# Optimization experiments

Measured on AMD Instinct MI355X. Metric: run time of the kernel, lower is better.

## Reference

```python
import jax, jax.numpy as jnp
import numpy as np

BN, BE, B = 50000, 800000, 16
NE, EE, GE, EH, NH = 32, 32, 32, 128, 128  # emb dims, hidden dims


def clean(x):
    return jnp.nan_to_num(x, nan=0.0, posinf=0.0, neginf=0.0)


def _lin(key, fan_in, fan_out):
    k1, k2 = jax.random.split(key)
    s = 1.0 / np.sqrt(fan_in)
    return (jax.random.uniform(k1, (fan_in, fan_out), jnp.float32, -s, s),
            jax.random.uniform(k2, (fan_out,), jnp.float32, -s, s))


def setup_inputs() -> dict:
    key = jax.random.key(0)
    ks = jax.random.split(key, 20)
    inp = {
        "x": jax.random.normal(ks[0], (BN, 2), jnp.float32),
        "edge_index": jax.random.randint(ks[1], (2, BE), 0, BN, jnp.int32),
        "batch": jax.random.randint(ks[2], (BN,), 0, B, jnp.int32),
        "node_attr": jnp.ones((BN, 2), jnp.float32),
        "edge_attr": jax.random.uniform(ks[3], (BE, 2), jnp.float32) + 0.5,  # positive spacings
        "glob_attr": jax.random.uniform(ks[4], (B, 2), jnp.float32),
    }
    # encoders (output 2*emb each, 'Duplicated')
    inp["enc_node_W"], inp["enc_node_b"] = _lin(ks[5], 2, 2 * NE)
    inp["enc_edge_W"], inp["enc_edge_b"] = _lin(ks[6], 2, 2 * EE)
    inp["enc_glob_W"], inp["enc_glob_b"] = _lin(ks[7], 2, 2 * GE)
    inp["enc2_W"], inp["enc2_b"] = _lin(ks[8], 2, 2 * EE)
    # derivative MLP: 4*NE+2*EE -> EH -> 2*EE
    inp["dW1"], inp["db1"] = _lin(ks[9], 4 * NE + 2 * EE, EH)
    inp["dW2"], inp["db2"] = _lin(ks[10], EH, 2 * EE)
    # half-jacobian MLP: 4*EE -> EH -> 2*EE
    inp["hW1"], inp["hb1"] = _lin(ks[11], 4 * EE, EH)
    inp["hW2"], inp["hb2"] = _lin(ks[12], EH, 2 * EE)
    # jacobian MLP: 6*EE -> NH -> 2*NE
    inp["jW1"], inp["jb1"] = _lin(ks[13], 6 * EE, NH)
    inp["jW2"], inp["jb2"] = _lin(ks[14], NH, 2 * NE)
    # hessian MLP: 4*EE+2*EE -> NH -> 2*NE
    inp["sW1"], inp["sb1"] = _lin(ks[15], 6 * EE, NH)
    inp["sW2"], inp["sb2"] = _lin(ks[16], NH, 2 * NE)
    # node MLP: 6*NE+2*GE -> NH -> 2*NE
    inp["nW1"], inp["nb1"] = _lin(ks[17], 6 * NE + 2 * GE, NH)
    inp["nW2"], inp["nb2"] = _lin(ks[18], NH, 2 * NE)
    # decoder: 2*NE -> 2
    inp["decW"], inp["decb"] = _lin(ks[19], 2 * NE, 2)
    return inp


def reference(x, edge_index, batch, node_attr, edge_attr, glob_attr,
              enc_node_W, enc_node_b, enc_edge_W, enc_edge_b, enc_glob_W, enc_glob_b,
              enc2_W, enc2_b,
              dW1, db1, dW2, db2,
              hW1, hb1, hW2, hb2,
              jW1, jb1, jW2, jb2,
              sW1, sb1, sW2, sb2,
              nW1, nb1, nW2, nb2,
              decW, decb):
    relu = jax.nn.relu
    seg = lambda d, idx: jax.ops.segment_sum(d, idx, num_segments=BN)
    mlp = lambda t, W1, b1, W2, b2: relu(t @ W1 + b1) @ W2 + b2

    row, col = edge_index[0], edge_index[1]
    spacing = edge_attr                                 # [BE,2]
    inv_spacing = clean(1.0 / spacing)
    inv_double = clean(1.0 / (seg(spacing, row) + seg(spacing, col)))  # [BN,2]

    node_emb = relu(x @ enc_node_W + enc_node_b)        # [BN,2*NE]
    spacing_emb = relu(spacing @ enc_edge_W + enc_edge_b)  # [BE,2*EE]
    glob_emb = relu(glob_attr @ enc_glob_W + enc_glob_b)   # [B,2*GE]
    inv_spacing_emb = relu(inv_spacing @ enc2_W + enc2_b)  # [BE,2*EE]
    inv_double_emb = relu(inv_double @ enc2_W + enc2_b)    # [BN,2*EE]

    d_edge = mlp(jnp.concatenate([node_emb[row], node_emb[col], inv_spacing_emb], -1),
                 dW1, db1, dW2, db2)                    # [BE,2*EE]
    hj_plus = seg(d_edge, row)                          # [BN,2*EE]
    hj_minus = seg(d_edge, col)

    jac1 = seg(mlp(jnp.concatenate([spacing_emb, hj_plus[col]], -1), hW1, hb1, hW2, hb2), col)
    jac2 = seg(mlp(jnp.concatenate([spacing_emb, hj_minus[row]], -1), hW1, hb1, hW2, hb2), row)
    jac = mlp(jnp.concatenate([jac1, jac2, inv_double_emb], -1), jW1, jb1, jW2, jb2)  # [BN,2*NE]

    hess = mlp(jnp.concatenate([hj_plus, hj_minus, inv_double_emb], -1), sW1, sb1, sW2, sb2)

    res = mlp(jnp.concatenate([node_emb, jac, glob_emb[batch], hess], -1), nW1, nb1, nW2, nb2)
    return node_attr * (res @ decW + decb)              # [BN,2]
```

## Files before the change

kernel.cpp:

```cpp
#include <hip/hip_runtime.h>
#include <hip/hip_fp16.h>
#include <math.h>

#define BN 50000
#define BE 800000
#define CHUNK 104

__device__ __forceinline__ float relu_f(float v) { return fmaxf(v, 0.0f); }
__device__ __forceinline__ float inv_clean(float s) {
    float q = 1.0f / s;
    return isfinite(q) ? q : 0.0f;
}
__device__ __forceinline__ float inv_clean_fast(float s) {
    float q = __builtin_amdgcn_rcpf(s);
    return isfinite(q) ? q : 0.0f;
}

__global__ __launch_bounds__(256) void k_pack_w1(
    const float* __restrict__ W, int r0, float4* __restrict__ dst)
{
    int t = blockIdx.x * 256 + threadIdx.x;
    if (t >= 2048) return;
    int j2 = t >> 6, l = t & 63;
    const float* ra = W + (size_t)(r0 + 2*j2) * 128 + 2*l;
    const float* rb = W + (size_t)(r0 + 2*j2 + 1) * 128 + 2*l;
    dst[t] = make_float4(ra[0], ra[1], rb[0], rb[1]);
}
__global__ __launch_bounds__(256) void k_pack_w2(
    const float* __restrict__ W2, float4* __restrict__ dst)
{
    int t = blockIdx.x * 256 + threadIdx.x;
    if (t >= 2048) return;
    int k4 = t >> 6, l = t & 63;
    dst[t] = make_float4(W2[(4*k4+0)*64+l], W2[(4*k4+1)*64+l],
                         W2[(4*k4+2)*64+l], W2[(4*k4+3)*64+l]);
}
__global__ __launch_bounds__(256) void k_pack_uv(
    const float* __restrict__ dW1, float4* __restrict__ dst)
{
    int t = blockIdx.x * 256 + threadIdx.x;
    if (t >= 4096) return;
    int j = t >> 6, l = t & 63;
    float4 w;
    if (l < 32) w = ((const float4*)(dW1 + (size_t)j*128))[l];
    else        w = ((const float4*)(dW1 + (size_t)(64+j)*128))[l-32];
    dst[t] = w;
}

__global__ __launch_bounds__(256) void k_hist_sumsp(
    const int* __restrict__ ei, const float* __restrict__ ea,
    int* __restrict__ rc, int* __restrict__ cc, float* __restrict__ sumsp)
{
    int e = blockIdx.x * 256 + threadIdx.x;
    if (e >= BE) return;
    int r = ei[e], c = ei[BE + e];
    atomicAdd(&rc[r], 1);
    atomicAdd(&cc[c], 1);
    float2 s = ((const float2*)ea)[e];
    atomicAdd(&sumsp[2*r],   s.x);
    atomicAdd(&sumsp[2*r+1], s.y);
    atomicAdd(&sumsp[2*c],   s.x);
    atomicAdd(&sumsp[2*c+1], s.y);
}

__global__ __launch_bounds__(1024) void k_scan(
    const int* __restrict__ cntR, int* __restrict__ hdR,
    const int* __restrict__ cntC, int* __restrict__ hdC)
{
    __shared__ int s[1024];
    const int* cnt; int* hd;
    if (blockIdx.x == 0) { cnt = cntR; hd = hdR; }
    else                 { cnt = cntC; hd = hdC; }
    int t = threadIdx.x;
    int base = t * 49;
    int sum = 0;
    for (int i = 0; i < 49; i++) {
        int idx = base + i;
        sum += (idx < BN) ? cnt[idx] : 0;
    }
    s[t] = sum;
    __syncthreads();
    for (int o = 1; o < 1024; o <<= 1) {
        int v = (t >= o) ? s[t - o] : 0;
        __syncthreads();
        s[t] += v;
        __syncthreads();
    }
    int run = s[t] - sum;
    for (int i = 0; i < 49; i++) {
        int idx = base + i;
        if (idx < BN) { hd[idx] = run; run += cnt[idx]; }
    }
}

__global__ __launch_bounds__(256) void k_scatter2(
    const int* __restrict__ ei, const float* __restrict__ ea,
    int* __restrict__ rhd, int* __restrict__ chd,
    int4* __restrict__ rs, int4* __restrict__ cs)
{
    int e = blockIdx.x * 256 + threadIdx.x;
    if (e >= BE) return;
    int r = ei[e], c = ei[BE + e];
    float2 s = ((const float2*)ea)[e];
    int s0 = __float_as_int(s.x), s1 = __float_as_int(s.y);
    int p1 = atomicAdd(&rhd[r], 1);
    rs[p1] = make_int4(r, c, s0, s1);
    int p2 = atomicAdd(&chd[c], 1);
    cs[p2] = make_int4(c, r, s0, s1);
}

__global__ __launch_bounds__(256, 6) void k_uvh(
    const float* __restrict__ x,
    const float* __restrict__ enW, const float* __restrict__ enB,
    const float4* __restrict__ guv,
    __half* __restrict__ u_h, __half* __restrict__ v_h)
{
    extern __shared__ float lds[];
    const int wid = threadIdx.x >> 6, l = threadIdx.x & 63;
    float4* xb4 = (float4*)(lds + wid * 512);
    const int gw = blockIdx.x * 4 + wid;
    const int nw = gridDim.x * 4;

    const int jj = l & 31;
    const float w0a = enW[jj],    w0b = enW[64+jj],  b0 = enB[jj];
    const float w1a = enW[jj+32], w1b = enW[96+jj],  b1 = enB[jj+32];

    for (int g = gw; g < BN/8; g += nw) {
        const int n0 = g * 8;
        const int q = l >> 5;
        {
            float2 xa = ((const float2*)x)[n0 + q*4 + 0];
            float2 xb = ((const float2*)x)[n0 + q*4 + 1];
            float2 xc = ((const float2*)x)[n0 + q*4 + 2];
            float2 xd = ((const float2*)x)[n0 + q*4 + 3];
            float4 p0, p1;
            p0.x = relu_f(fmaf(xa.x, w0a, fmaf(xa.y, w0b, b0)));
            p0.y = relu_f(fmaf(xb.x, w0a, fmaf(xb.y, w0b, b0)));
            p0.z = relu_f(fmaf(xc.x, w0a, fmaf(xc.y, w0b, b0)));
            p0.w = relu_f(fmaf(xd.x, w0a, fmaf(xd.y, w0b, b0)));
            p1.x = relu_f(fmaf(xa.x, w1a, fmaf(xa.y, w1b, b1)));
            p1.y = relu_f(fmaf(xb.x, w1a, fmaf(xb.y, w1b, b1)));
// ... 7 lines not shown
        for (int e = 0; e < 8; e++) acc[e] = make_float4(0,0,0,0);
        #pragma unroll 8
        for (int j = 0; j < 64; j++) {
            float4 wq = guv[j*64 + l];
            float4 xa = xb4[j*2 + 0];
            float4 xc = xb4[j*2 + 1];
            acc[0].x = fmaf(xa.x, wq.x, acc[0].x); acc[0].y = fmaf(xa.x, wq.y, acc[0].y);
            acc[0].z = fmaf(xa.x, wq.z, acc[0].z); acc[0].w = fmaf(xa.x, wq.w, acc[0].w);
            acc[1].x = fmaf(xa.y, wq.x, acc[1].x); acc[1].y = fmaf(xa.y, wq.y, acc[1].y);
            acc[1].z = fmaf(xa.y, wq.z, acc[1].z); acc[1].w = fmaf(xa.y, wq.w, acc[1].w);
            acc[2].x = fmaf(xa.z, wq.x, acc[2].x); acc[2].y = fmaf(xa.z, wq.y, acc[2].y);
            acc[2].z = fmaf(xa.z, wq.z, acc[2].z); acc[2].w = fmaf(xa.z, wq.w, acc[2].w);
            acc[3].x = fmaf(xa.w, wq.x, acc[3].x); acc[3].y = fmaf(xa.w, wq.y, acc[3].y);
            acc[3].z = fmaf(xa.w, wq.z, acc[3].z); acc[3].w = fmaf(xa.w, wq.w, acc[3].w);
            acc[4].x = fmaf(xc.x, wq.x, acc[4].x); acc[4].y = fmaf(xc.x, wq.y, acc[4].y);
            acc[4].z = fmaf(xc.x, wq.z, acc[4].z); acc[4].w = fmaf(xc.x, wq.w, acc[4].w);
            acc[5].x = fmaf(xc.y, wq.x, acc[5].x); acc[5].y = fmaf(xc.y, wq.y, acc[5].y);
            acc[5].z = fmaf(xc.y, wq.z, acc[5].z); acc[5].w = fmaf(xc.y, wq.w, acc[5].w);
            acc[6].x = fmaf(xc.z, wq.x, acc[6].x); acc[6].y = fmaf(xc.z, wq.y, acc[6].y);
            acc[6].z = fmaf(xc.z, wq.z, acc[6].z); acc[6].w = fmaf(xc.z, wq.w, acc[6].w);
            acc[7].x = fmaf(xc.w, wq.x, acc[7].x); acc[7].y = fmaf(xc.w, wq.y, acc[7].y);
            acc[7].z = fmaf(xc.w, wq.z, acc[7].z); acc[7].w = fmaf(xc.w, wq.w, acc[7].w);
        }
        __half* dst = (l < 32) ? (u_h + 4*l) : (v_h + 4*(l-32));
        #pragma unroll
        for (int e = 0; e < 8; e++) {
            __half2* p = (__half2*)(dst + (size_t)(n0+e)*128);
            p[0] = __floats2half2_rn(acc[e].x, acc[e].y);
            p[1] = __floats2half2_rn(acc[e].z, acc[e].w);
        }
    }
}

__global__ __launch_bounds__(256, 8) void k_e1s(
    const int4* __restrict__ rs,
    const __half* __restrict__ u_h, const __half* __restrict__ v_h,
    const float* __restrict__ e2w, const float* __restrict__ e2b,
    const float4* __restrict__ gw1, const float* __restrict__ db1,
    const float4* __restrict__ gw2, const float* __restrict__ db2,
    float* __restrict__ hjp, float* __restrict__ hjm)
{
    extern __shared__ float lds[];
    const int wid = threadIdx.x >> 6, l = threadIdx.x & 63;
    float* buf = lds + wid * 1024;
    float4* buf4 = (float4*)buf;

    const int jA = l >> 1;
    const int eh = l & 1;
    const float ewA0 = e2w[jA],      ewB0 = e2w[64+jA],    eb0v = e2b[jA];
    const float ewA1 = e2w[jA+32],   ewB1 = e2w[96+jA],    eb1v = e2b[jA+32];
    const float b1a = db1[2*l], b1b = db1[2*l+1];
    const float b2r = db2[l];

    const int wave = blockIdx.x * 4 + wid;
    const int start = wave * CHUNK;
    const int end = min(start + CHUNK, BE);

    float acc = 0.f;
    int cur = -1;

    for (int i = start; i < end; i += 8) {
        const int nact = min(8, end - i);
        int rr[8], cc[8];
        float2 spv[8];
        #pragma unroll
        for (int e = 0; e < 8; e++) {
            int idx = i + ((e < nact) ? e : nact - 1);
            int4 rec = rs[idx];
            rr[e] = rec.x; cc[e] = rec.y;
            spv[e] = make_float2(__int_as_float(rec.z), __int_as_float(rec.w));
        }
        {
            float2 sA = eh ? spv[4] : spv[0];
            float2 sB = eh ? spv[5] : spv[1];
            float2 sC = eh ? spv[6] : spv[2];
            float2 sD = eh ? spv[7] : spv[3];
            float qA0 = inv_clean_fast(sA.x), qA1 = inv_clean_fast(sA.y);
            float qB0 = inv_clean_fast(sB.x), qB1 = inv_clean_fast(sB.y);
            float qC0 = inv_clean_fast(sC.x), qC1 = inv_clean_fast(sC.y);
            float qD0 = inv_clean_fast(sD.x), qD1 = inv_clean_fast(sD.y);
            float4 p0, p1;
            p0.x = relu_f(fmaf(qA0, ewA0, fmaf(qA1, ewB0, eb0v)));
            p0.y = relu_f(fmaf(qB0, ewA0, fmaf(qB1, ewB0, eb0v)));
            p0.z = relu_f(fmaf(qC0, ewA0, fmaf(qC1, ewB0, eb0v)));
            p0.w = relu_f(fmaf(qD0, ewA0, fmaf(qD1, ewB0, eb0v)));
            p1.x = relu_f(fmaf(qA0, ewA1, fmaf(qA1, ewB1, eb1v)));
            p1.y = relu_f(fmaf(qB0, ewA1, fmaf(qB1, ewB1, eb1v)));
            p1.z = relu_f(fmaf(qC0, ewA1, fmaf(qC1, ewB1, eb1v)));
            p1.w = relu_f(fmaf(qD0, ewA1, fmaf(qD1, ewB1, eb1v)));
            buf4[jA*2 + eh]      = p0;
            buf4[(jA+32)*2 + eh] = p1;
        }

        float t0[8], t1[8];
        #pragma unroll
        for (int e = 0; e < 8; e++) {
            float2 uu = __half22float2(*(const __half2*)(u_h + (size_t)rr[e]*128 + 2*l));
            float2 vv = __half22float2(*(const __half2*)(v_h + (size_t)cc[e]*128 + 2*l));
            t0[e] = b1a + uu.x + vv.x;
            t1[e] = b1b + uu.y + vv.y;
        }

        #pragma unroll 8
        for (int j2 = 0; j2 < 32; j2++) {
            float4 wq = gw1[j2*64 + l];
            float4 xa = buf4[(2*j2)*2 + 0];
            float4 xbv = buf4[(2*j2)*2 + 1];
            float4 xc = buf4[(2*j2+1)*2 + 0];
            float4 xd = buf4[(2*j2+1)*2 + 1];
            t0[0] = fmaf(xa.x, wq.x, fmaf(xc.x, wq.z, t0[0]));
            t1[0] = fmaf(xa.x, wq.y, fmaf(xc.x, wq.w, t1[0]));
            t0[1] = fmaf(xa.y, wq.x, fmaf(xc.y, wq.z, t0[1]));
            t1[1] = fmaf(xa.y, wq.y, fmaf(xc.y, wq.w, t1[1]));
            t0[2] = fmaf(xa.z, wq.x, fmaf(xc.z, wq.z, t0[2]));
            t1[2] = fmaf(xa.z, wq.y, fmaf(xc.z, wq.w, t1[2]));
            t0[3] = fmaf(xa.w, wq.x, fmaf(xc.w, wq.z, t0[3]));
            t1[3] = fmaf(xa.w, wq.y, fmaf(xc.w, wq.w, t1[3]));
            t0[4] = fmaf(xbv.x, wq.x, fmaf(xd.x, wq.z, t0[4]));
            t1[4] = fmaf(xbv.x, wq.y, fmaf(xd.x, wq.w, t1[4]));
            t0[5] = fmaf(xbv.y, wq.x, fmaf(xd.y, wq.z, t0[5]));
            t1[5] = fmaf(xbv.y, wq.y, fmaf(xd.y, wq.w, t1[5]));
            t0[6] = fmaf(xbv.z, wq.x, fmaf(xd.z, wq.z, t0[6]));
            t1[6] = fmaf(xbv.z, wq.y, fmaf(xd.z, wq.w, t1[6]));
            t0[7] = fmaf(xbv.w, wq.x, fmaf(xd.w, wq.z, t0[7]));
            t1[7] = fmaf(xbv.w, wq.y, fmaf(xd.w, wq.w, t1[7]));
        }

        #pragma unroll
        for (int e = 0; e < 8; e++) {
            *(float2*)(buf + e*128 + 2*l) = make_float2(relu_f(t0[e]), relu_f(t1[e]));
        }
        float o[8] = {0,0,0,0,0,0,0,0};
        #pragma unroll 8
        for (int k4 = 0; k4 < 32; k4++) {
            float4 wq = gw2[k4*64 + l];
            #pragma unroll
            for (int e = 0; e < 8; e++) {
                float4 hb = *(const float4*)(buf + e*128 + 4*k4);
                o[e] = fmaf(hb.x, wq.x, fmaf(hb.y, wq.y,
                        fmaf(hb.z, wq.z, fmaf(hb.w, wq.w, o[e]))));
            }
        }
        #pragma unroll
        for (int e = 0; e < 8; e++) {
            if (e < nact) {
                float ov = o[e] + b2r;
                atomicAdd(&hjm[(size_t)cc[e]*64 + l], ov);
                if (rr[e] != cur) {
                    if (cur >= 0) atomicAdd(&hjp[(size_t)cur*64 + l], acc);
                    acc = 0.f;
                    cur = rr[e];
                }
                acc += ov;
            }
        }
    }
    if (cur >= 0) atomicAdd(&hjp[(size_t)cur*64 + l], acc);
}

__global__ __launch_bounds__(256, 6) void k_tptmh(
    const float* __restrict__ hjp, const float* __restrict__ hjm,
    const float4* __restrict__ gtp,
    __half* __restrict__ tp_h, __half* __restrict__ tm_h)
{
    extern __shared__ float lds[];
    const int wid = threadIdx.x >> 6, l = threadIdx.x & 63;
    float4* xb4 = (float4*)(lds + wid * 512);
    const int gw = blockIdx.x * 4 + wid;
    const int nw = gridDim.x * 4;
    const int NG = BN/8;

    for (int vg = gw; vg < 2*NG; vg += nw) {
        const float* in = (vg < NG) ? hjp : hjm;
        __half*     out = (vg < NG) ? tp_h : tm_h;
        const int n0 = ((vg < NG) ? vg : vg - NG) * 8;
        const int q = l >> 5;
        #pragma unroll
        for (int r = 0; r < 2; r++) {
            int j = (l & 31) + 32*r;
            float v0 = in[(n0 + q*4 + 0)*64 + j];
            float v1 = in[(n0 + q*4 + 1)*64 + j];
            float v2 = in[(n0 + q*4 + 2)*64 + j];
            float v3 = in[(n0 + q*4 + 3)*64 + j];
            xb4[j*2 + q] = make_float4(v0, v1, v2, v3);
        }
        float a0[8] = {0,0,0,0,0,0,0,0}, a1[8] = {0,0,0,0,0,0,0,0};
        #pragma unroll 8
        for (int j2 = 0; j2 < 32; j2++) {
            float4 wq = gtp[j2*64 + l];
            float4 xa = xb4[(2*j2)*2 + 0];
            float4 xbv = xb4[(2*j2)*2 + 1];
            float4 xc = xb4[(2*j2+1)*2 + 0];
            float4 xd = xb4[(2*j2+1)*2 + 1];
            a0[0] = fmaf(xa.x, wq.x, fmaf(xc.x, wq.z, a0[0]));
            a1[0] = fmaf(xa.x, wq.y, fmaf(xc.x, wq.w, a1[0]));
            a0[1] = fmaf(xa.y, wq.x, fmaf(xc.y, wq.z, a0[1]));
            a1[1] = fmaf(xa.y, wq.y, fmaf(xc.y, wq.w, a1[1]));
            a0[2] = fmaf(xa.z, wq.x, fmaf(xc.z, wq.z, a0[2]));
            a1[2] = fmaf(xa.z, wq.y, fmaf(xc.z, wq.w, a1[2]));
            a0[3] = fmaf(xa.w, wq.x, fmaf(xc.w, wq.z, a0[3]));
            a1[3] = fmaf(xa.w, wq.y, fmaf(xc.w, wq.w, a1[3]));
            a0[4] = fmaf(xbv.x, wq.x, fmaf(xd.x, wq.z, a0[4]));
            a1[4] = fmaf(xbv.x, wq.y, fmaf(xd.x, wq.w, a1[4]));
            a0[5] = fmaf(xbv.y, wq.x, fmaf(xd.y, wq.z, a0[5]));
            a1[5] = fmaf(xbv.y, wq.y, fmaf(xd.y, wq.w, a1[5]));
            a0[6] = fmaf(xbv.z, wq.x, fmaf(xd.z, wq.z, a0[6]));
            a1[6] = fmaf(xbv.z, wq.y, fmaf(xd.z, wq.w, a1[6]));
            a0[7] = fmaf(xbv.w, wq.x, fmaf(xd.w, wq.z, a0[7]));
            a1[7] = fmaf(xbv.w, wq.y, fmaf(xd.w, wq.w, a1[7]));
        }
        #pragma unroll
        for (int e = 0; e < 8; e++) {
            *(__half2*)(out + (size_t)(n0+e)*128 + 2*l) = __floats2half2_rn(a0[e], a1[e]);
        }
    }
}

__global__ __launch_bounds__(256, 8) void k_e2s(
    const int4* __restrict__ data, const __half* __restrict__ tvals_h,
    const float* __restrict__ eew, const float* __restrict__ eeb,
    const float4* __restrict__ gw1, const float* __restrict__ hb1,
    const float4* __restrict__ gw2, const float* __restrict__ hb2,
    float* __restrict__ out)
{
    extern __shared__ float lds[];
    const int wid = threadIdx.x >> 6, l = threadIdx.x & 63;
    float* buf = lds + wid * 1024;
    float4* buf4 = (float4*)buf;

    const int jA = l >> 1;
    const int eh = l & 1;
    const float ewA0 = eew[jA],    ewB0 = eew[64+jA],  eb0v = eeb[jA];
    const float ewA1 = eew[jA+32], ewB1 = eew[96+jA],  eb1v = eeb[jA+32];
    const float b1a = hb1[2*l], b1b = hb1[2*l+1];
    const float b2r = hb2[l];

    const int wave = blockIdx.x * 4 + wid;
    const int start = wave * CHUNK;
    const int end = min(start + CHUNK, BE);

    float acc = 0.f;
    int cur = -1;

    for (int i = start; i < end; i += 8) {
        const int nact = min(8, end - i);
        int kk[8];
        float2 spv[8];
        #pragma unroll
        for (int e = 0; e < 8; e++) {
            int idx = i + ((e < nact) ? e : nact - 1);
            int4 rec = data[idx];
            kk[e] = rec.x;
            spv[e] = make_float2(__int_as_float(rec.z), __int_as_float(rec.w));
        }
        {
            float2 sA = eh ? spv[4] : spv[0];
            float2 sB = eh ? spv[5] : spv[1];
            float2 sC = eh ? spv[6] : spv[2];
            float2 sD = eh ? spv[7] : spv[3];
            float4 p0, p1;
            p0.x = relu_f(fmaf(sA.x, ewA0, fmaf(sA.y, ewB0, eb0v)));
            p0.y = relu_f(fmaf(sB.x, ewA0, fmaf(sB.y, ewB0, eb0v)));
            p0.z = relu_f(fmaf(sC.x, ewA0, fmaf(sC.y, ewB0, eb0v)));
            p0.w = relu_f(fmaf(sD.x, ewA0, fmaf(sD.y, ewB0, eb0v)));
            p1.x = relu_f(fmaf(sA.x, ewA1, fmaf(sA.y, ewB1, eb1v)));
            p1.y = relu_f(fmaf(sB.x, ewA1, fmaf(sB.y, ewB1, eb1v)));
            p1.z = relu_f(fmaf(sC.x, ewA1, fmaf(sC.y, ewB1, eb1v)));
            p1.w = relu_f(fmaf(sD.x, ewA1, fmaf(sD.y, ewB1, eb1v)));
            buf4[jA*2 + eh]      = p0;
            buf4[(jA+32)*2 + eh] = p1;
        }

        float2 tv[8];
        #pragma unroll
        for (int e = 0; e < 8; e++)
            tv[e] = __half22float2(*(const __half2*)(tvals_h + (size_t)kk[e]*128 + 2*l));

        float t0[8], t1[8];
        #pragma unroll
        for (int e = 0; e < 8; e++) { t0[e] = b1a; t1[e] = b1b; }

        #pragma unroll 8
        for (int j2 = 0; j2 < 32; j2++) {
            float4 wq = gw1[j2*64 + l];
            float4 xa = buf4[(2*j2)*2 + 0];
            float4 xbv = buf4[(2*j2)*2 + 1];
            float4 xc = buf4[(2*j2+1)*2 + 0];
            float4 xd = buf4[(2*j2+1)*2 + 1];
            t0[0] = fmaf(xa.x, wq.x, fmaf(xc.x, wq.z, t0[0]));
            t1[0] = fmaf(xa.x, wq.y, fmaf(xc.x, wq.w, t1[0]));
            t0[1] = fmaf(xa.y, wq.x, fmaf(xc.y, wq.z, t0[1]));
            t1[1] = fmaf(xa.y, wq.y, fmaf(xc.y, wq.w, t1[1]));
            t0[2] = fmaf(xa.z, wq.x, fmaf(xc.z, wq.z, t0[2]));
            t1[2] = fmaf(xa.z, wq.y, fmaf(xc.z, wq.w, t1[2]));
            t0[3] = fmaf(xa.w, wq.x, fmaf(xc.w, wq.z, t0[3]));
            t1[3] = fmaf(xa.w, wq.y, fmaf(xc.w, wq.w, t1[3]));
            t0[4] = fmaf(xbv.x, wq.x, fmaf(xd.x, wq.z, t0[4]));
            t1[4] = fmaf(xbv.x, wq.y, fmaf(xd.x, wq.w, t1[4]));
            t0[5] = fmaf(xbv.y, wq.x, fmaf(xd.y, wq.z, t0[5]));
            t1[5] = fmaf(xbv.y, wq.y, fmaf(xd.y, wq.w, t1[5]));
            t0[6] = fmaf(xbv.z, wq.x, fmaf(xd.z, wq.z, t0[6]));
            t1[6] = fmaf(xbv.z, wq.y, fmaf(xd.z, wq.w, t1[6]));
            t0[7] = fmaf(xbv.w, wq.x, fmaf(xd.w, wq.z, t0[7]));
            t1[7] = fmaf(xbv.w, wq.y, fmaf(xd.w, wq.w, t1[7]));
        }

        #pragma unroll
        for (int e = 0; e < 8; e++) {
            *(float2*)(buf + e*128 + 2*l) =
                make_float2(relu_f(t0[e] + tv[e].x), relu_f(t1[e] + tv[e].y));
        }
        float o[8] = {0,0,0,0,0,0,0,0};
        #pragma unroll 8
        for (int k4 = 0; k4 < 32; k4++) {
            float4 wq = gw2[k4*64 + l];
            #pragma unroll
            for (int e = 0; e < 8; e++) {
                float4 hb = *(const float4*)(buf + e*128 + 4*k4);
                o[e] = fmaf(hb.x, wq.x, fmaf(hb.y, wq.y,
                         fmaf(hb.z, wq.z, fmaf(hb.w, wq.w, o[e]))));
            }
        }
        #pragma unroll
        for (int e = 0; e < 8; e++) {
            if (e < nact) {
                float val = o[e] + b2r;
                if (kk[e] != cur) {
                    if (cur >= 0) atomicAdd(&out[(size_t)cur*64 + l], acc);
                    acc = 0.f;
                    cur = kk[e];
                }
                acc += val;
            }
        }
    }
    if (cur >= 0) atomicAdd(&out[(size_t)cur*64 + l], acc);
}

__global__ __launch_bounds__(256, 4) void k_node_mlp(
    const float* __restrict__ A, const float* __restrict__ Bv,
    const float* __restrict__ sumsp,
    const float* __restrict__ e2w_g, const float* __restrict__ e2b_g,
    const float* __restrict__ W1g, const float* __restrict__ b1g,
    const float* __restrict__ W2g, const float* __restrict__ b2g,
    float* __restrict__ outp)
{
    extern __shared__ float lds[];
    const int wid = threadIdx.x >> 6, l = threadIdx.x & 63;
    float* xbuf = lds + wid * 768;
    float* hbuf = lds + 4*768 + wid * 512;

    const float ewl = e2w_g[l], ewl2 = e2w_g[64+l], ebl = e2b_g[l];
    const float bb0 = b1g[2*l], bb1 = b1g[2*l+1];
    const float bo = b2g[l];

    const int gw = blockIdx.x * 4 + wid;
    const int nw = gridDim.x * 4;

    for (int g = gw; g < BN/4; g += nw) {
        const int i0 = g * 4;
        float av[4], bv[4], iv[4];
        #pragma unroll
        for (int e = 0; e < 4; e++) {
// ... 144 lines not shown
    const float* enc_glob_W = (const float*)d_in[10];
    const float* enc_glob_b = (const float*)d_in[11];
    const float* enc2_W     = (const float*)d_in[12];
    const float* enc2_b     = (const float*)d_in[13];
    const float* dW1 = (const float*)d_in[14]; const float* db1 = (const float*)d_in[15];
    const float* dW2 = (const float*)d_in[16]; const float* db2 = (const float*)d_in[17];
    const float* hW1 = (const float*)d_in[18]; const float* hb1 = (const float*)d_in[19];
    const float* hW2 = (const float*)d_in[20]; const float* hb2 = (const float*)d_in[21];
    const float* jW1 = (const float*)d_in[22]; const float* jb1 = (const float*)d_in[23];
    const float* jW2 = (const float*)d_in[24]; const float* jb2 = (const float*)d_in[25];
    const float* sW1 = (const float*)d_in[26]; const float* sb1 = (const float*)d_in[27];
    const float* sW2 = (const float*)d_in[28]; const float* sb2 = (const float*)d_in[29];
    const float* nW1 = (const float*)d_in[30]; const float* nb1 = (const float*)d_in[31];
    const float* nW2 = (const float*)d_in[32]; const float* nb2 = (const float*)d_in[33];
    const float* decW = (const float*)d_in[34]; const float* decb = (const float*)d_in[35];

    float* ws = (float*)d_ws;
    int4*   rs    = (int4*)ws;
    int4*   cs    = (int4*)(ws + 3200000);
    __half* u_h   = (__half*)(ws + 6400000);
    __half* v_h   = (__half*)(ws + 9600000);
    float*  hjp   = ws + 12800000;
    float*  hjm   = ws + 16000000;
    float*  jac1  = ws + 19200000;
    float*  jac2  = ws + 22400000;
    float*  sumsp = ws + 25600000;
    int*    row_cnt = (int*)(ws + 25700000);
    int*    col_cnt = row_cnt + 50176;
    int*    row_hd  = col_cnt + 50176;
    int*    col_hd  = row_hd + 50048;

    float* scratch = (float*)d_out;
    float4* puv   = (float4*)(scratch);
    float4* pw1e1 = (float4*)(scratch + 16384);
    float4* pw2e1 = (float4*)(scratch + 24576);
    float4* pw1tp = (float4*)(scratch + 32768);
    float4* pw1e2 = (float4*)(scratch + 40960);
    float4* pw2e2 = (float4*)(scratch + 49152);

    hipMemsetAsync(hjp, 0, (size_t)12800000*sizeof(float), stream);
    hipMemsetAsync(sumsp, 0, (size_t)(100000 + 2*50176)*sizeof(float), stream);

    k_pack_uv<<<16, 256, 0, stream>>>(dW1, puv);
    k_pack_w1<<<8, 256, 0, stream>>>(dW1, 128, pw1e1);
    k_pack_w2<<<8, 256, 0, stream>>>(dW2, pw2e1);
    k_pack_w1<<<8, 256, 0, stream>>>(hW1, 64, pw1tp);
    k_pack_w1<<<8, 256, 0, stream>>>(hW1, 0, pw1e2);
    k_pack_w2<<<8, 256, 0, stream>>>(hW2, pw2e2);

    k_uvh<<<1563, 256, 2048*4, stream>>>(x, enc_node_W, enc_node_b, puv, u_h, v_h);

    k_hist_sumsp<<<3125, 256, 0, stream>>>(ei, edge_attr, row_cnt, col_cnt, sumsp);
    k_scan<<<2, 1024, 0, stream>>>(row_cnt, row_hd, col_cnt, col_hd);
    k_scatter2<<<3125, 256, 0, stream>>>(ei, edge_attr, row_hd, col_hd, rs, cs);

    const int E_BLOCKS = ((BE + CHUNK - 1) / CHUNK + 3) / 4;
    k_e1s<<<E_BLOCKS, 256, 4096*4, stream>>>(rs, u_h, v_h, enc2_W, enc2_b,
                                             pw1e1, db1, pw2e1, db2, hjp, hjm);

    k_tptmh<<<1536, 256, 2048*4, stream>>>(hjp, hjm, pw1tp, u_h, v_h);

    k_e2s<<<E_BLOCKS, 256, 4096*4, stream>>>(cs, u_h, enc_edge_W, enc_edge_b,
                                             pw1e2, hb1, pw2e2, hb2, jac1);
    k_e2s<<<E_BLOCKS, 256, 4096*4, stream>>>(rs, v_h, enc_edge_W, enc_edge_b,
                                             pw1e2, hb1, pw2e2, hb2, jac2);

    size_t lds_nm = (4*768 + 4*512) * sizeof(float);
    k_node_mlp<<<1024, 256, lds_nm, stream>>>(jac1, jac2, sumsp, enc2_W, enc2_b,
                                              jW1, jb1, jW2, jb2, jac1);
    k_node_mlp<<<1024, 256, lds_nm, stream>>>(hjp, hjm, sumsp, enc2_W, enc2_b,
                                              sW1, sb1, sW2, sb2, hjp);

    size_t lds_nf = (4*1024 + 4*512) * sizeof(float);
    k_node_final<<<1024, 256, lds_nf, stream>>>(x, enc_node_W, enc_node_b,
                                                jac1, hjp,
                                                batch, glob_attr, enc_glob_W, enc_glob_b,
                                                nW1, nb1, nW2, nb2, decW, decb,
                                                node_attr, (float*)d_out);
}
```

Before: 2.588 ms.

## Use fp16 dot2 for edge MLPs, split edge kernel, compute sumsp via CSR

Edge MLP weights and activations are packed to fp16 and the matmuls use v_dot2 fp16 instructions with fp32 accumulation, halving LDS and weight traffic and halving the FMA count. The first edge kernel is split into two passes over row-sorted and column-sorted records, so both hj_plus and hj_minus get run-length-merged atomics instead of per-edge atomics for hjm. The float atomic spacing sums are replaced by a per-node CSR reduction after scatter. This costs an extra full edge pass and lowers intermediate precision to fp16.

```diff
diff --git a/kernel.cpp b/kernel.cpp
--- a/kernel.cpp
+++ b/kernel.cpp
@@ -5,6 +5,8 @@
 #define BN 50000
 #define BE 800000
 #define CHUNK 104
+
+typedef _Float16 h2 __attribute__((ext_vector_type(2)));
 
 __device__ __forceinline__ float relu_f(float v) { return fmaxf(v, 0.0f); }
 __device__ __forceinline__ float inv_clean(float s) {
@@ -14,6 +16,14 @@
 __device__ __forceinline__ float inv_clean_fast(float s) {
     float q = __builtin_amdgcn_rcpf(s);
     return isfinite(q) ? q : 0.0f;
+}
+__device__ __forceinline__ float fdot2f(h2 a, h2 b, float c) {
+    return __builtin_amdgcn_fdot2(a, b, c, false);
+}
+__device__ __forceinline__ unsigned int h2u(h2 v) { union { h2 h; unsigned int u; } x; x.h = v; return x.u; }
+__device__ __forceinline__ h2 uh2(unsigned int v) { union { unsigned int u; h2 h; } x; x.u = v; return x.h; }
+__device__ __forceinline__ unsigned int packh2(float a, float b) {
+    h2 h; h.x = (_Float16)a; h.y = (_Float16)b; return h2u(h);
 }
 
 __global__ __launch_bounds__(256) void k_pack_w1(
@@ -25,15 +35,6 @@
     const float* ra = W + (size_t)(r0 + 2*j2) * 128 + 2*l;
     const float* rb = W + (size_t)(r0 + 2*j2 + 1) * 128 + 2*l;
     dst[t] = make_float4(ra[0], ra[1], rb[0], rb[1]);
-}
-__global__ __launch_bounds__(256) void k_pack_w2(
-    const float* __restrict__ W2, float4* __restrict__ dst)
-{
-    int t = blockIdx.x * 256 + threadIdx.x;
-    if (t >= 2048) return;
-    int k4 = t >> 6, l = t & 63;
-    dst[t] = make_float4(W2[(4*k4+0)*64+l], W2[(4*k4+1)*64+l],
-                         W2[(4*k4+2)*64+l], W2[(4*k4+3)*64+l]);
 }
 __global__ __launch_bounds__(256) void k_pack_uv(
     const float* __restrict__ dW1, float4* __restrict__ dst)
@@ -46,21 +47,34 @@
     else        w = ((const float4*)(dW1 + (size_t)(64+j)*128))[l-32];
     dst[t] = w;
 }
-
-__global__ __launch_bounds__(256) void k_hist_sumsp(
-    const int* __restrict__ ei, const float* __restrict__ ea,
-    int* __restrict__ rc, int* __restrict__ cc, float* __restrict__ sumsp)
+__global__ __launch_bounds__(256) void k_pack_w1h(
+    const float* __restrict__ W, int r0, uint2* __restrict__ dst)
+{
+    int t = blockIdx.x * 256 + threadIdx.x;
+    if (t >= 2048) return;
+    int j2 = t >> 6, l = t & 63;
+    const float* ra = W + (size_t)(r0 + 2*j2) * 128;
+    const float* rb = W + (size_t)(r0 + 2*j2 + 1) * 128;
+    dst[t] = make_uint2(packh2(ra[2*l],   rb[2*l]),
+                        packh2(ra[2*l+1], rb[2*l+1]));
+}
+__global__ __launch_bounds__(256) void k_pack_w2h(
+    const float* __restrict__ W2, uint2* __restrict__ dst)
+{
+    int t = blockIdx.x * 256 + threadIdx.x;
+    if (t >= 2048) return;
+    int k4 = t >> 6, l = t & 63;
+    dst[t] = make_uint2(packh2(W2[(4*k4+0)*64+l], W2[(4*k4+1)*64+l]),
+                        packh2(W2[(4*k4+2)*64+l], W2[(4*k4+3)*64+l]));
+}
+
+__global__ __launch_bounds__(256) void k_hist(
+    const int* __restrict__ ei, int* __restrict__ rc, int* __restrict__ cc)
 {
     int e = blockIdx.x * 256 + threadIdx.x;
     if (e >= BE) return;
-    int r = ei[e], c = ei[BE + e];
-    atomicAdd(&rc[r], 1);
-    atomicAdd(&cc[c], 1);
-    float2 s = ((const float2*)ea)[e];
-    atomicAdd(&sumsp[2*r],   s.x);
-    atomicAdd(&sumsp[2*r+1], s.y);
-    atomicAdd(&sumsp[2*c],   s.x);
-    atomicAdd(&sumsp[2*c+1], s.y);
+    atomicAdd(&rc[ei[e]], 1);
+    atomicAdd(&cc[ei[BE + e]], 1);
 }
 
 __global__ __launch_bounds__(1024) void k_scan(
@@ -107,6 +121,28 @@
     rs[p1] = make_int4(r, c, s0, s1);
     int p2 = atomicAdd(&chd[c], 1);
     cs[p2] = make_int4(c, r, s0, s1);
+}
+
+__global__ __launch_bounds__(256) void k_sumsp2(
+    const int4* __restrict__ rs, const int* __restrict__ rhd, const int* __restrict__ rcnt,
+    const int4* __restrict__ cs, const int* __restrict__ chd, const int* __restrict__ ccnt,
+    float* __restrict__ sumsp)
+{
+    int n = blockIdx.x * 256 + threadIdx.x;
+    if (n >= BN) return;
+    float s0 = 0.f, s1 = 0.f;
+    int e1 = rhd[n], e0 = e1 - rcnt[n];
+    for (int j = e0; j < e1; j++) {
+        int4 rec = rs[j];
+        s0 += __int_as_float(rec.z); s1 += __int_as_float(rec.w);
+    }
+    e1 = chd[n]; e0 = e1 - ccnt[n];
+    for (int j = e0; j < e1; j++) {
+        int4 rec = cs[j];
+        s0 += __int_as_float(rec.z); s1 += __int_as_float(rec.w);
+    }
+    sumsp[2*n]   = s0;
+    sumsp[2*n+1] = s1;
 }
 
 __global__ __launch_bounds__(256, 6) void k_uvh(
@@ -180,23 +216,22 @@
     }
 }
 
-__global__ __launch_bounds__(256, 8) void k_e1s(
-    const int4* __restrict__ rs,
-    const __half* __restrict__ u_h, const __half* __restrict__ v_h,
+__global__ __launch_bounds__(256, 8) void k_e1d(
+    const int4* __restrict__ recs,
+    const __half* __restrict__ A_h, const __half* __restrict__ B_h,
     const float* __restrict__ e2w, const float* __restrict__ e2b,
-    const float4* __restrict__ gw1, const float* __restrict__ db1,
-    const float4* __restrict__ gw2, const float* __restrict__ db2,
-    float* __restrict__ hjp, float* __restrict__ hjm)
-{
-    extern __shared__ float lds[];
+    const uint2* __restrict__ pw1, const float* __restrict__ db1,
+    const uint2* __restrict__ pw2, const float* __restrict__ db2,
+    float* __restrict__ outAcc)
+{
+    extern __shared__ unsigned int ldsu[];
     const int wid = threadIdx.x >> 6, l = threadIdx.x & 63;
-    float* buf = lds + wid * 1024;
-    float4* buf4 = (float4*)buf;
-
-    const int jA = l >> 1;
-    const int eh = l & 1;
-    const float ewA0 = e2w[jA],      ewB0 = e2w[64+jA],    eb0v = e2b[jA];
-    const float ewA1 = e2w[jA+32],   ewB1 = e2w[96+jA],    eb1v = e2b[jA+32];
+    uint4* xbuf = (uint4*)ldsu + (size_t)wid * 192;
+    uint4* hbuf = xbuf + 64;
+
+    const int j2 = l >> 1, eh = l & 1;
+    const float w0a = e2w[2*j2],    w0b = e2w[64+2*j2], eb0 = e2b[2*j2];
+    const float w1a = e2w[2*j2+1],  w1b = e2w[65+2*j2], eb1 = e2b[2*j2+1];
     const float b1a = db1[2*l], b1b = db1[2*l+1];
     const float b2r = db2[l];
 
@@ -209,101 +244,96 @@
 
     for (int i = start; i < end; i += 8) {
         const int nact = min(8, end - i);
-        int rr[8], cc[8];
-        float2 spv[8];
+        int key[8], oth[8];
+        float spx[8], spy[8];
         #pragma unroll
         for (int e = 0; e < 8; e++) {
             int idx = i + ((e < nact) ? e : nact - 1);
-            int4 rec = rs[idx];
-            rr[e] = rec.x; cc[e] = rec.y;
-            spv[e] = make_float2(__int_as_float(rec.z), __int_as_float(rec.w));
+            int4 rec = recs[idx];
+            key[e] = rec.x; oth[e] = rec.y;
+            spx[e] = __int_as_float(rec.z); spy[e] = __int_as_float(rec.w);
         }
         {
-            float2 sA = eh ? spv[4] : spv[0];
-            float2 sB = eh ? spv[5] : spv[1];
-            float2 sC = eh ? spv[6] : spv[2];
-            float2 sD = eh ? spv[7] : spv[3];
-            float qA0 = inv_clean_fast(sA.x), qA1 = inv_clean_fast(sA.y);
-            float qB0 = inv_clean_fast(sB.x), qB1 = inv_clean_fast(sB.y);
-            float qC0 = inv_clean_fast(sC.x), qC1 = inv_clean_fast(sC.y);
-            float qD0 = inv_clean_fast(sD.x), qD1 = inv_clean_fast(sD.y);
-            float4 p0, p1;
-            p0.x = relu_f(fmaf(qA0, ewA0, fmaf(qA1, ewB0, eb0v)));
-            p0.y = relu_f(fmaf(qB0, ewA0, fmaf(qB1, ewB0, eb0v)));
-            p0.z = relu_f(fmaf(qC0, ewA0, fmaf(qC1, ewB0, eb0v)));
-            p0.w = relu_f(fmaf(qD0, ewA0, fmaf(qD1, ewB0, eb0v)));
-            p1.x = relu_f(fmaf(qA0, ewA1, fmaf(qA1, ewB1, eb1v)));
-            p1.y = relu_f(fmaf(qB0, ewA1, fmaf(qB1, ewB1, eb1v)));
-            p1.z = relu_f(fmaf(qC0, ewA1, fmaf(qC1, ewB1, eb1v)));
-            p1.w = relu_f(fmaf(qD0, ewA1, fmaf(qD1, ewB1, eb1v)));
-            buf4[jA*2 + eh]      = p0;
-            buf4[(jA+32)*2 + eh] = p1;
-        }
-
+            uint4 xw;
+            unsigned int* xp = (unsigned int*)&xw;
+            #pragma unroll
+            for (int c = 0; c < 4; c++) {
+                int e = 4*eh + c;
+                float q0 = inv_clean_fast(spx[e]);
+                float q1 = inv_clean_fast(spy[e]);
+                float r0 = relu_f(fmaf(q0, w0a, fmaf(q1, w0b, eb0)));
+                float r1 = relu_f(fmaf(q0, w1a, fmaf(q1, w1b, eb1)));
+                xp[c] = packh2(r0, r1);
+            }
+            xbuf[j2*2 + eh] = xw;
+        }
         float t0[8], t1[8];
         #pragma unroll
         for (int e = 0; e < 8; e++) {
-            float2 uu = __half22float2(*(const __half2*)(u_h + (size_t)rr[e]*128 + 2*l));
-            float2 vv = __half22float2(*(const __half2*)(v_h + (size_t)cc[e]*128 + 2*l));
-            t0[e] = b1a + uu.x + vv.x;
-            t1[e] = b1b + uu.y + vv.y;
-        }
-
-        #pragma unroll 8
-        for (int j2 = 0; j2 < 32; j2++) {
-            float4 wq = gw1[j2*64 + l];
-            float4 xa = buf4[(2*j2)*2 + 0];
-            float4 xbv = buf4[(2*j2)*2 + 1];
-            float4 xc = buf4[(2*j2+1)*2 + 0];
-            float4 xd = buf4[(2*j2+1)*2 + 1];
-            t0[0] = fmaf(xa.x, wq.x, fmaf(xc.x, wq.z, t0[0]));
-            t1[0] = fmaf(xa.x, wq.y, fmaf(xc.x, wq.w, t1[0]));
-            t0[1] = fmaf(xa.y, wq.x, fmaf(xc.y, wq.z, t0[1]));
-            t1[1] = fmaf(xa.y, wq.y, fmaf(xc.y, wq.w, t1[1]));
-            t0[2] = fmaf(xa.z, wq.x, fmaf(xc.z, wq.z, t0[2]));
-            t1[2] = fmaf(xa.z, wq.y, fmaf(xc.z, wq.w, t1[2]));
-            t0[3] = fmaf(xa.w, wq.x, fmaf(xc.w, wq.z, t0[3]));
-            t1[3] = fmaf(xa.w, wq.y, fmaf(xc.w, wq.w, t1[3]));
-            t0[4] = fmaf(xbv.x, wq.x, fmaf(xd.x, wq.z, t0[4]));
-            t1[4] = fmaf(xbv.x, wq.y, fmaf(xd.x, wq.w, t1[4]));
-            t0[5] = fmaf(xbv.y, wq.x, fmaf(xd.y, wq.z, t0[5]));
-            t1[5] = fmaf(xbv.y, wq.y, fmaf(xd.y, wq.w, t1[5]));
-            t0[6] = fmaf(xbv.z, wq.x, fmaf(xd.z, wq.z, t0[6]));
-            t1[6] = fmaf(xbv.z, wq.y, fmaf(xd.z, wq.w, t1[6]));
-            t0[7] = fmaf(xbv.w, wq.x, fmaf(xd.w, wq.z, t0[7]));
-            t1[7] = fmaf(xbv.w, wq.y, fmaf(xd.w, wq.w, t1[7]));
-        }
-
-        #pragma unroll
-        for (int e = 0; e < 8; e++) {
-            *(float2*)(buf + e*128 + 2*l) = make_float2(relu_f(t0[e]), relu_f(t1[e]));
+            float2 au = __half22float2(*(const __half2*)(A_h + (size_t)key[e]*128 + 2*l));
+            float2 bu = __half22float2(*(const __half2*)(B_h + (size_t)oth[e]*128 + 2*l));
+            t0[e] = b1a + au.x + bu.x;
+            t1[e] = b1b + au.y + bu.y;
+        }
+        #pragma unroll 8
+        for (int p = 0; p < 32; p++) {
+            uint4 x0 = xbuf[p*2 + 0];
+            uint4 x1 = xbuf[p*2 + 1];
+            uint2 wv = pw1[p*64 + l];
+            h2 wa = uh2(wv.x), wb = uh2(wv.y);
+            t0[0] = fdot2f(uh2(x0.x), wa, t0[0]); t1[0] = fdot2f(uh2(x0.x), wb, t1[0]);
+            t0[1] = fdot2f(uh2(x0.y), wa, t0[1]); t1[1] = fdot2f(uh2(x0.y), wb, t1[1]);
+            t0[2] = fdot2f(uh2(x0.z), wa, t0[2]); t1[2] = fdot2f(uh2(x0.z), wb, t1[2]);
+            t0[3] = fdot2f(uh2(x0.w), wa, t0[3]); t1[3] = fdot2f(uh2(x0.w), wb, t1[3]);
+            t0[4] = fdot2f(uh2(x1.x), wa, t0[4]); t1[4] = fdot2f(uh2(x1.x), wb, t1[4]);
+            t0[5] = fdot2f(uh2(x1.y), wa, t0[5]); t1[5] = fdot2f(uh2(x1.y), wb, t1[5]);
+            t0[6] = fdot2f(uh2(x1.z), wa, t0[6]); t1[6] = fdot2f(uh2(x1.z), wb, t1[6]);
+            t0[7] = fdot2f(uh2(x1.w), wa, t0[7]); t1[7] = fdot2f(uh2(x1.w), wb, t1[7]);
+        }
+        {
+            uint4 hA, hB;
+            unsigned int* pa = (unsigned int*)&hA;
+            unsigned int* pb = (unsigned int*)&hB;
+            #pragma unroll
+            for (int c = 0; c < 4; c++) {
+                pa[c] = packh2(relu_f(t0[c]),   relu_f(t1[c]));
+                pb[c] = packh2(relu_f(t0[4+c]), relu_f(t1[4+c]));
+            }
+            hbuf[l*2 + 0] = hA;
+            hbuf[l*2 + 1] = hB;
         }
         float o[8] = {0,0,0,0,0,0,0,0};
         #pragma unroll 8
         for (int k4 = 0; k4 < 32; k4++) {
-            float4 wq = gw2[k4*64 + l];
-            #pragma unroll
-            for (int e = 0; e < 8; e++) {
-                float4 hb = *(const float4*)(buf + e*128 + 4*k4);
-                o[e] = fmaf(hb.x, wq.x, fmaf(hb.y, wq.y,
-                        fmaf(hb.z, wq.z, fmaf(hb.w, wq.w, o[e]))));
-            }
+            uint4 a0 = hbuf[(2*k4)*2 + 0];
+            uint4 a1 = hbuf[(2*k4)*2 + 1];
+            uint4 b0 = hbuf[(2*k4+1)*2 + 0];
+            uint4 b1 = hbuf[(2*k4+1)*2 + 1];
+            uint2 wv = pw2[k4*64 + l];
+            h2 wa = uh2(wv.x), wb = uh2(wv.y);
+            o[0] = fdot2f(uh2(b0.x), wb, fdot2f(uh2(a0.x), wa, o[0]));
+            o[1] = fdot2f(uh2(b0.y), wb, fdot2f(uh2(a0.y), wa, o[1]));
+            o[2] = fdot2f(uh2(b0.z), wb, fdot2f(uh2(a0.z), wa, o[2]));
+            o[3] = fdot2f(uh2(b0.w), wb, fdot2f(uh2(a0.w), wa, o[3]));
+            o[4] = fdot2f(uh2(b1.x), wb, fdot2f(uh2(a1.x), wa, o[4]));
+            o[5] = fdot2f(uh2(b1.y), wb, fdot2f(uh2(a1.y), wa, o[5]));
+            o[6] = fdot2f(uh2(b1.z), wb, fdot2f(uh2(a1.z), wa, o[6]));
+            o[7] = fdot2f(uh2(b1.w), wb, fdot2f(uh2(a1.w), wa, o[7]));
         }
         #pragma unroll
         for (int e = 0; e < 8; e++) {
             if (e < nact) {
-                float ov = o[e] + b2r;
-                atomicAdd(&hjm[(size_t)cc[e]*64 + l], ov);
-                if (rr[e] != cur) {
-                    if (cur >= 0) atomicAdd(&hjp[(size_t)cur*64 + l], acc);
+                float val = o[e] + b2r;
+                if (key[e] != cur) {
+                    if (cur >= 0) atomicAdd(&outAcc[(size_t)cur*64 + l], acc);
                     acc = 0.f;
-                    cur = rr[e];
+                    cur = key[e];
                 }
-                acc += ov;
+                acc += val;
             }
         }
     }
-    if (cur >= 0) atomicAdd(&hjp[(size_t)cur*64 + l], acc);
+    if (cur >= 0) atomicAdd(&outAcc[(size_t)cur*64 + l], acc);
 }
 
 __global__ __launch_bounds__(256, 6) void k_tptmh(
@@ -365,21 +395,20 @@
 }
 
 __global__ __launch_bounds__(256, 8) void k_e2s(
-    const int4* __restrict__ data, const __half* __restrict__ tvals_h,
+    const int4* __restrict__ recs, const __half* __restrict__ tvals_h,
     const float* __restrict__ eew, const float* __restrict__ eeb,
-    const float4* __restrict__ gw1, const float* __restrict__ hb1,
-    const float4* __restrict__ gw2, const float* __restrict__ hb2,
+    const uint2* __restrict__ pw1, const float* __restrict__ hb1,
+    const uint2* __restrict__ pw2, const float* __restrict__ hb2,
     float* __restrict__ out)
 {
-    extern __shared__ float lds[];
+    extern __shared__ unsigned int ldsu[];
     const int wid = threadIdx.x >> 6, l = threadIdx.x & 63;
-    float* buf = lds + wid * 1024;
-    float4* buf4 = (float4*)buf;
-
-    const int jA = l >> 1;
-    const int eh = l & 1;
-    const float ewA0 = eew[jA],    ewB0 = eew[64+jA],  eb0v = eeb[jA];
-    const float ewA1 = eew[jA+32], ewB1 = eew[96+jA],  eb1v = eeb[jA+32];
+    uint4* xbuf = (uint4*)ldsu + (size_t)wid * 192;
+    uint4* hbuf = xbuf + 64;
+
+    const int j2 = l >> 1, eh = l & 1;
+    const float w0a = eew[2*j2],    w0b = eew[64+2*j2], eb0 = eeb[2*j2];
+    const float w1a = eew[2*j2+1],  w1b = eew[65+2*j2], eb1 = eeb[2*j2+1];
     const float b1a = hb1[2*l], b1b = hb1[2*l+1];
     const float b2r = hb2[l];
 
@@ -392,91 +421,87 @@
 
     for (int i = start; i < end; i += 8) {
         const int nact = min(8, end - i);
-        int kk[8];
-        float2 spv[8];
+        int key[8];
+        float spx[8], spy[8];
         #pragma unroll
         for (int e = 0; e < 8; e++) {
             int idx = i + ((e < nact) ? e : nact - 1);
-            int4 rec = data[idx];
-            kk[e] = rec.x;
-            spv[e] = make_float2(__int_as_float(rec.z), __int_as_float(rec.w));
+            int4 rec = recs[idx];
+            key[e] = rec.x;
+            spx[e] = __int_as_float(rec.z); spy[e] = __int_as_float(rec.w);
         }
         {
-            float2 sA = eh ? spv[4] : spv[0];
-            float2 sB = eh ? spv[5] : spv[1];
-            float2 sC = eh ? spv[6] : spv[2];
-            float2 sD = eh ? spv[7] : spv[3];
-            float4 p0, p1;
-            p0.x = relu_f(fmaf(sA.x, ewA0, fmaf(sA.y, ewB0, eb0v)));
-            p0.y = relu_f(fmaf(sB.x, ewA0, fmaf(sB.y, ewB0, eb0v)));
-            p0.z = relu_f(fmaf(sC.x, ewA0, fmaf(sC.y, ewB0, eb0v)));
-            p0.w = relu_f(fmaf(sD.x, ewA0, fmaf(sD.y, ewB0, eb0v)));
-            p1.x = relu_f(fmaf(sA.x, ewA1, fmaf(sA.y, ewB1, eb1v)));
-            p1.y = relu_f(fmaf(sB.x, ewA1, fmaf(sB.y, ewB1, eb1v)));
-            p1.z = relu_f(fmaf(sC.x, ewA1, fmaf(sC.y, ewB1, eb1v)));
-            p1.w = relu_f(fmaf(sD.x, ewA1, fmaf(sD.y, ewB1, eb1v)));
-            buf4[jA*2 + eh]      = p0;
-            buf4[(jA+32)*2 + eh] = p1;
-        }
-
-        float2 tv[8];
-        #pragma unroll
-        for (int e = 0; e < 8; e++)
-            tv[e] = __half22float2(*(const __half2*)(tvals_h + (size_t)kk[e]*128 + 2*l));
-
+            uint4 xw;
+            unsigned int* xp = (unsigned int*)&xw;
+            #pragma unroll
+            for (int c = 0; c < 4; c++) {
+                int e = 4*eh + c;
+                float r0 = relu_f(fmaf(spx[e], w0a, fmaf(spy[e], w0b, eb0)));
+                float r1 = relu_f(fmaf(spx[e], w1a, fmaf(spy[e], w1b, eb1)));
+                xp[c] = packh2(r0, r1);
+            }
+            xbuf[j2*2 + eh] = xw;
+        }
         float t0[8], t1[8];
         #pragma unroll
-        for (int e = 0; e < 8; e++) { t0[e] = b1a; t1[e] = b1b; }
-
-        #pragma unroll 8
-        for (int j2 = 0; j2 < 32; j2++) {
-            float4 wq = gw1[j2*64 + l];
-            float4 xa = buf4[(2*j2)*2 + 0];
-            float4 xbv = buf4[(2*j2)*2 + 1];
-            float4 xc = buf4[(2*j2+1)*2 + 0];
-            float4 xd = buf4[(2*j2+1)*2 + 1];
-            t0[0] = fmaf(xa.x, wq.x, fmaf(xc.x, wq.z, t0[0]));
-            t1[0] = fmaf(xa.x, wq.y, fmaf(xc.x, wq.w, t1[0]));
-            t0[1] = fmaf(xa.y, wq.x, fmaf(xc.y, wq.z, t0[1]));
-            t1[1] = fmaf(xa.y, wq.y, fmaf(xc.y, wq.w, t1[1]));
-            t0[2] = fmaf(xa.z, wq.x, fmaf(xc.z, wq.z, t0[2]));
-            t1[2] = fmaf(xa.z, wq.y, fmaf(xc.z, wq.w, t1[2]));
-            t0[3] = fmaf(xa.w, wq.x, fmaf(xc.w, wq.z, t0[3]));
-            t1[3] = fmaf(xa.w, wq.y, fmaf(xc.w, wq.w, t1[3]));
-            t0[4] = fmaf(xbv.x, wq.x, fmaf(xd.x, wq.z, t0[4]));
-            t1[4] = fmaf(xbv.x, wq.y, fmaf(xd.x, wq.w, t1[4]));
-            t0[5] = fmaf(xbv.y, wq.x, fmaf(xd.y, wq.z, t0[5]));
-            t1[5] = fmaf(xbv.y, wq.y, fmaf(xd.y, wq.w, t1[5]));
-            t0[6] = fmaf(xbv.z, wq.x, fmaf(xd.z, wq.z, t0[6]));
-            t1[6] = fmaf(xbv.z, wq.y, fmaf(xd.z, wq.w, t1[6]));
-            t0[7] = fmaf(xbv.w, wq.x, fmaf(xd.w, wq.z, t0[7]));
-            t1[7] = fmaf(xbv.w, wq.y, fmaf(xd.w, wq.w, t1[7]));
-        }
-
-        #pragma unroll
         for (int e = 0; e < 8; e++) {
-            *(float2*)(buf + e*128 + 2*l) =
-                make_float2(relu_f(t0[e] + tv[e].x), relu_f(t1[e] + tv[e].y));
+            float2 tv = __half22float2(*(const __half2*)(tvals_h + (size_t)key[e]*128 + 2*l));
+            t0[e] = b1a + tv.x;
+            t1[e] = b1b + tv.y;
+        }
+        #pragma unroll 8
+        for (int p = 0; p < 32; p++) {
+            uint4 x0 = xbuf[p*2 + 0];
+            uint4 x1 = xbuf[p*2 + 1];
+            uint2 wv = pw1[p*64 + l];
+            h2 wa = uh2(wv.x), wb = uh2(wv.y);
+            t0[0] = fdot2f(uh2(x0.x), wa, t0[0]); t1[0] = fdot2f(uh2(x0.x), wb, t1[0]);
+            t0[1] = fdot2f(uh2(x0.y), wa, t0[1]); t1[1] = fdot2f(uh2(x0.y), wb, t1[1]);
+            t0[2] = fdot2f(uh2(x0.z), wa, t0[2]); t1[2] = fdot2f(uh2(x0.z), wb, t1[2]);
+            t0[3] = fdot2f(uh2(x0.w), wa, t0[3]); t1[3] = fdot2f(uh2(x0.w), wb, t1[3]);
+            t0[4] = fdot2f(uh2(x1.x), wa, t0[4]); t1[4] = fdot2f(uh2(x1.x), wb, t1[4]);
+            t0[5] = fdot2f(uh2(x1.y), wa, t0[5]); t1[5] = fdot2f(uh2(x1.y), wb, t1[5]);
+            t0[6] = fdot2f(uh2(x1.z), wa, t0[6]); t1[6] = fdot2f(uh2(x1.z), wb, t1[6]);
+            t0[7] = fdot2f(uh2(x1.w), wa, t0[7]); t1[7] = fdot2f(uh2(x1.w), wb, t1[7]);
+        }
+        {
+            uint4 hA, hB;
+            unsigned int* pa = (unsigned int*)&hA;
+            unsigned int* pb = (unsigned int*)&hB;
+            #pragma unroll
+            for (int c = 0; c < 4; c++) {
+                pa[c] = packh2(relu_f(t0[c]),   relu_f(t1[c]));
+                pb[c] = packh2(relu_f(t0[4+c]), relu_f(t1[4+c]));
+            }
+            hbuf[l*2 + 0] = hA;
+            hbuf[l*2 + 1] = hB;
         }
         float o[8] = {0,0,0,0,0,0,0,0};
         #pragma unroll 8
         for (int k4 = 0; k4 < 32; k4++) {
-            float4 wq = gw2[k4*64 + l];
-            #pragma unroll
-            for (int e = 0; e < 8; e++) {
-                float4 hb = *(const float4*)(buf + e*128 + 4*k4);
-                o[e] = fmaf(hb.x, wq.x, fmaf(hb.y, wq.y,
-                         fmaf(hb.z, wq.z, fmaf(hb.w, wq.w, o[e]))));
-            }
+            uint4 a0 = hbuf[(2*k4)*2 + 0];
+            uint4 a1 = hbuf[(2*k4)*2 + 1];
+            uint4 b0 = hbuf[(2*k4+1)*2 + 0];
+            uint4 b1 = hbuf[(2*k4+1)*2 + 1];
+            uint2 wv = pw2[k4*64 + l];
+            h2 wa = uh2(wv.x), wb = uh2(wv.y);
+            o[0] = fdot2f(uh2(b0.x), wb, fdot2f(uh2(a0.x), wa, o[0]));
+            o[1] = fdot2f(uh2(b0.y), wb, fdot2f(uh2(a0.y), wa, o[1]));
+            o[2] = fdot2f(uh2(b0.z), wb, fdot2f(uh2(a0.z), wa, o[2]));
+            o[3] = fdot2f(uh2(b0.w), wb, fdot2f(uh2(a0.w), wa, o[3]));
+            o[4] = fdot2f(uh2(b1.x), wb, fdot2f(uh2(a1.x), wa, o[4]));
+            o[5] = fdot2f(uh2(b1.y), wb, fdot2f(uh2(a1.y), wa, o[5]));
+            o[6] = fdot2f(uh2(b1.z), wb, fdot2f(uh2(a1.z), wa, o[6]));
+            o[7] = fdot2f(uh2(b1.w), wb, fdot2f(uh2(a1.w), wa, o[7]));
         }
         #pragma unroll
         for (int e = 0; e < 8; e++) {
             if (e < nact) {
                 float val = o[e] + b2r;
-                if (kk[e] != cur) {
+                if (key[e] != cur) {
                     if (cur >= 0) atomicAdd(&out[(size_t)cur*64 + l], acc);
                     acc = 0.f;
-                    cur = kk[e];
+                    cur = key[e];
                 }
                 acc += val;
             }
@@ -687,38 +712,43 @@
 
     float* scratch = (float*)d_out;
     float4* puv   = (float4*)(scratch);
-    float4* pw1e1 = (float4*)(scratch + 16384);
-    float4* pw2e1 = (float4*)(scratch + 24576);
-    float4* pw1tp = (float4*)(scratch + 32768);
-    float4* pw1e2 = (float4*)(scratch + 40960);
-    float4* pw2e2 = (float4*)(scratch + 49152);
+    float4* ptp   = (float4*)(scratch + 16384);
+    uint2*  pe1w1 = (uint2*)(scratch + 24576);
+    uint2*  pe1w2 = (uint2*)(scratch + 28672);
+    uint2*  pe2w1 = (uint2*)(scratch + 32768);
+    uint2*  pe2w2 = (uint2*)(scratch + 36864);
 
     hipMemsetAsync(hjp, 0, (size_t)12800000*sizeof(float), stream);
-    hipMemsetAsync(sumsp, 0, (size_t)(100000 + 2*50176)*sizeof(float), stream);
+    hipMemsetAsync(row_cnt, 0, (size_t)(2*50176)*sizeof(int), stream);
 
     k_pack_uv<<<16, 256, 0, stream>>>(dW1, puv);
-    k_pack_w1<<<8, 256, 0, stream>>>(dW1, 128, pw1e1);
-    k_pack_w2<<<8, 256, 0, stream>>>(dW2, pw2e1);
-    k_pack_w1<<<8, 256, 0, stream>>>(hW1, 64, pw1tp);
-    k_pack_w1<<<8, 256, 0, stream>>>(hW1, 0, pw1e2);
-    k_pack_w2<<<8, 256, 0, stream>>>(hW2, pw2e2);
+    k_pack_w1<<<8, 256, 0, stream>>>(hW1, 64, ptp);
+    k_pack_w1h<<<8, 256, 0, stream>>>(dW1, 128, pe1w1);
+    k_pack_w2h<<<8, 256, 0, stream>>>(dW2, pe1w2);
+    k_pack_w1h<<<8, 256, 0, stream>>>(hW1, 0, pe2w1);
+    k_pack_w2h<<<8, 256, 0, stream>>>(hW2, pe2w2);
 
     k_uvh<<<1563, 256, 2048*4, stream>>>(x, enc_node_W, enc_node_b, puv, u_h, v_h);
 
-    k_hist_sumsp<<<3125, 256, 0, stream>>>(ei, edge_attr, row_cnt, col_cnt, sumsp);
+    k_hist<<<3125, 256, 0, stream>>>(ei, row_cnt, col_cnt);
     k_scan<<<2, 1024, 0, stream>>>(row_cnt, row_hd, col_cnt, col_hd);
     k_scatter2<<<3125, 256, 0, stream>>>(ei, edge_attr, row_hd, col_hd, rs, cs);
+    k_sumsp2<<<196, 256, 0, stream>>>(rs, row_hd, row_cnt, cs, col_hd, col_cnt, sumsp);
 
     const int E_BLOCKS = ((BE + CHUNK - 1) / CHUNK + 3) / 4;
-    k_e1s<<<E_BLOCKS, 256, 4096*4, stream>>>(rs, u_h, v_h, enc2_W, enc2_b,
-                                             pw1e1, db1, pw2e1, db2, hjp, hjm);
-
-    k_tptmh<<<1536, 256, 2048*4, stream>>>(hjp, hjm, pw1tp, u_h, v_h);
-
-    k_e2s<<<E_BLOCKS, 256, 4096*4, stream>>>(cs, u_h, enc_edge_W, enc_edge_b,
-                                             pw1e2, hb1, pw2e2, hb2, jac1);
-    k_e2s<<<E_BLOCKS, 256, 4096*4, stream>>>(rs, v_h, enc_edge_W, enc_edge_b,
-                                             pw1e2, hb1, pw2e2, hb2, jac2);
+    const size_t lds_e = 4 * 192 * 16;
+
+    k_e1d<<<E_BLOCKS, 256, lds_e, stream>>>(rs, u_h, v_h, enc2_W, enc2_b,
+                                            pe1w1, db1, pe1w2, db2, hjp);
+    k_e1d<<<E_BLOCKS, 256, lds_e, stream>>>(cs, v_h, u_h, enc2_W, enc2_b,
+                                            pe1w1, db1, pe1w2, db2, hjm);
+
+    k_tptmh<<<1536, 256, 2048*4, stream>>>(hjp, hjm, ptp, u_h, v_h);
+
+    k_e2s<<<E_BLOCKS, 256, lds_e, stream>>>(cs, u_h, enc_edge_W, enc_edge_b,
+                                            pe2w1, hb1, pe2w2, hb2, jac1);
+    k_e2s<<<E_BLOCKS, 256, lds_e, stream>>>(rs, v_h, enc_edge_W, enc_edge_b,
+                                            pe2w1, hb1, pe2w2, hb2, jac2);
 
     size_t lds_nm = (4*768 + 4*512) * sizeof(float);
     k_node_mlp<<<1024, 256, lds_nm, stream>>>(jac1, jac2, sumsp, enc2_W, enc2_b,
```

Measured after the change: 2.435 ms. 5.9% less time.
